# Kernel tuning notes

Measured on AMD Instinct MI355X. Metric: run time of the kernel, lower is better.

The kernel has to match this reference:

```python
import jax, jax.numpy as jnp
import numpy as np

TOP_K = 1
N_EXPERTS = 32
ALPHA = 0.001
SCALING = 1.0


def setup_inputs() -> dict:
    key = jax.random.key(0)
    k1, k2 = jax.random.split(key)
    hidden_states = jax.random.normal(k1, (16, 8192, 256), dtype=jnp.float32)
    # kaiming_uniform-ish gate weight, scale irrelevant for correctness check
    weight = jax.random.normal(k2, (32, 256), dtype=jnp.float32) * 0.06
    return {"hidden_states": hidden_states, "weight": weight}


def reference(hidden_states, weight):
    bsz, seq_len, h = hidden_states.shape
    x = hidden_states.reshape(-1, h).astype(jnp.float32)           # [N, h]
    logits = jnp.einsum('nh,eh->ne', x, weight.astype(jnp.float32))  # [N, E]
    scores = jax.nn.softmax(logits, axis=-1)
    # greedy top-k (sorted order fine; torch uses sorted=False but values identical for k=1)
    topk_weight, topk_idx = jax.lax.top_k(scores, TOP_K)            # [N, K]
    topk_weight = topk_weight * SCALING  # norm_topk_prob=False, top_k=1
    # seq_aux loss (training branch, alpha > 0)
    idx_aux = topk_idx.reshape(bsz, seq_len * TOP_K)                # [B, S*K]
    ce = jax.vmap(lambda idx: jnp.zeros((N_EXPERTS,), jnp.float32).at[idx].add(1.0))(idx_aux)
    ce = ce / (seq_len * TOP_K / N_EXPERTS)
    scores_seq = scores.reshape(bsz, seq_len, N_EXPERTS)
    aux_loss = jnp.mean(jnp.sum(ce * jnp.mean(scores_seq, axis=1), axis=1)) * ALPHA
    return topk_idx, topk_weight, aux_loss
```

## Files before the change

### kernel.cpp

```cpp
#include <hip/hip_runtime.h>
#include <math.h>

#define NTOK (16 * 8192)
#define H    256
#define E    32
#define SEQ  8192
#define BSZ  16

#define FOR_E(M) M(0) M(1) M(2) M(3) M(4) M(5) M(6) M(7) \
                 M(8) M(9) M(10) M(11) M(12) M(13) M(14) M(15) \
                 M(16) M(17) M(18) M(19) M(20) M(21) M(22) M(23) \
                 M(24) M(25) M(26) M(27) M(28) M(29) M(30) M(31)

__device__ __forceinline__ float waveReduceSum(float v) {
#pragma unroll
    for (int off = 32; off > 0; off >>= 1) v += __shfl_xor(v, off, 64);
    return v;
}

__global__ __launch_bounds__(256) void zero_ws_kernel(float* ws) {
    int i = blockIdx.x * 256 + threadIdx.x;
    if (i < BSZ * E * 2) ws[i] = 0.0f;
}

__global__ __launch_bounds__(256, 2) void gate_kernel(
    const float* __restrict__ x, const float* __restrict__ w,
    float* __restrict__ out, float* __restrict__ ws_cnt, float* __restrict__ ws_sum)
{
    __shared__ float w_lds[E * H];

    const int tid = threadIdx.x;

    {
        float4*       wl = (float4*)w_lds;
        const float4* wg = (const float4*)w;
#pragma unroll
        for (int i = 0; i < (E * H / 4) / 256; ++i)
            wl[tid + 256 * i] = wg[tid + 256 * i];
    }
    __syncthreads();

    const int lane = tid & 63;
    const int col  = lane & 31;
    const int half = lane >> 5;
    const int wavebase = blockIdx.x * 256 + (tid >> 6) * 64;
    const int tok0 = wavebase + col * 2;

    const float* xb = x + (size_t)tok0 * H + half * 128;
    const float* wb = w_lds + half * 128;

#define DECL_ACC(e) float aA##e = 0.0f, aB##e = 0.0f;
    FOR_E(DECL_ACC)

    float4 cA0 = *(const float4*)(xb);
    float4 cA1 = *(const float4*)(xb + 4);
    float4 cB0 = *(const float4*)(xb + H);
    float4 cB1 = *(const float4*)(xb + H + 4);

#pragma unroll 1
    for (int hc = 0; hc < 128; hc += 8) {
        const int hn = (hc + 8) & 127;
        const float4 nA0 = *(const float4*)(xb + hn);
        const float4 nA1 = *(const float4*)(xb + hn + 4);
        const float4 nB0 = *(const float4*)(xb + H + hn);
        const float4 nB1 = *(const float4*)(xb + H + hn + 4);

#define FMA_E(e) { \
        const float4 w0 = *(const float4*)(wb + (e) * H + hc); \
        const float4 w1 = *(const float4*)(wb + (e) * H + hc + 4); \
        float ta = aA##e, tb = aB##e; \
        ta = fmaf(w0.x, cA0.x, ta); ta = fmaf(w0.y, cA0.y, ta); \
        ta = fmaf(w0.z, cA0.z, ta); ta = fmaf(w0.w, cA0.w, ta); \
        ta = fmaf(w1.x, cA1.x, ta); ta = fmaf(w1.y, cA1.y, ta); \
        ta = fmaf(w1.z, cA1.z, ta); ta = fmaf(w1.w, cA1.w, ta); \
        tb = fmaf(w0.x, cB0.x, tb); tb = fmaf(w0.y, cB0.y, tb); \
        tb = fmaf(w0.z, cB0.z, tb); tb = fmaf(w0.w, cB0.w, tb); \
        tb = fmaf(w1.x, cB1.x, tb); tb = fmaf(w1.y, cB1.y, tb); \
        tb = fmaf(w1.z, cB1.z, tb); tb = fmaf(w1.w, cB1.w, tb); \
        aA##e = ta; aB##e = tb; }
        FOR_E(FMA_E)

        cA0 = nA0; cA1 = nA1; cB0 = nB0; cB1 = nB1;
    }

#define RED_E(e) aA##e += __shfl_xor(aA##e, 32, 64); aB##e += __shfl_xor(aB##e, 32, 64);
    FOR_E(RED_E)

#define SEL_E(e) const float L##e = half ? aB##e : aA##e;
    FOR_E(SEL_E)

    float m  = -3.402823466e+38f;
    int   id = 0;
#define AMAX_E(e) if (L##e > m) { m = L##e; id = (e); }
    FOR_E(AMAX_E)

    float ss = 0.0f;
#define EXP_E(e) const float p##e = __expf(L##e - m); ss += p##e;
    FOR_E(EXP_E)

    const float inv = 1.0f / ss;
    const int token = tok0 + half;
    out[token]        = (float)id;
    out[NTOK + token] = inv;

    const int b = wavebase >> 13;

#define AUX_E(e) { \
        const float sc = waveReduceSum(p##e * inv); \
        const unsigned long long bl = __ballot(id == (e)); \
        if (lane == 0) { \
            atomicAdd(&ws_sum[b * E + (e)], sc); \
            const float cn = (float)__popcll(bl); \
            if (cn != 0.0f) atomicAdd(&ws_cnt[b * E + (e)], cn); \
        } }
    FOR_E(AUX_E)
}

__global__ __launch_bounds__(256) void aux_kernel(
    const float* __restrict__ ws_cnt, const float* __restrict__ ws_sum,
    float* __restrict__ out)
{
    const int tid = threadIdx.x;
    float p = 0.0f;
    for (int i = tid; i < BSZ * E; i += 256)
        p += ws_cnt[i] * ws_sum[i];

    __shared__ float red[4];
#pragma unroll
    for (int off = 32; off > 0; off >>= 1)
        p += __shfl_xor(p, off, 64);
    if ((tid & 63) == 0) red[tid >> 6] = p;
    __syncthreads();
    if (tid == 0) {
        float t = red[0] + red[1] + red[2] + red[3];
        out[2 * NTOK] = t * (0.001f / (16.0f * 256.0f * 8192.0f));
    }
}

extern "C" void kernel_launch(void* const* d_in, const int* in_sizes, int n_in,
                              void* d_out, int out_size, void* d_ws, size_t ws_size,
                              hipStream_t stream) {
    const float* x = (const float*)d_in[0];
    const float* w = (const float*)d_in[1];
    float* out    = (float*)d_out;
    float* ws     = (float*)d_ws;
    float* ws_cnt = ws;
    float* ws_sum = ws + BSZ * E;

    zero_ws_kernel<<<4, 256, 0, stream>>>(ws);
    gate_kernel<<<NTOK / 256, 256, 0, stream>>>(x, w, out, ws_cnt, ws_sum);
    aux_kernel<<<1, 256, 0, stream>>>(ws_cnt, ws_sum, out);
}
```

Measured before the change: 261.4 us.

## Map one token per thread, read gate weights from global, aggregate aux stats in LDS

Each thread now computes the full 256-dim dot products for one token instead of splitting the hidden dimension across half-waves, which removes the cross-lane shuffle reduction. The gate weight is read straight from global memory (wave-uniform addresses, so likely scalar/cached loads) instead of being staged into 32KB of LDS, freeing LDS and raising possible occupancy. Per-block aux sums and counts are gathered in shared memory first, so each block issues only 32 global atomics per array. The trade-off is a strided per-thread row access pattern for x (each lane reads a different 1KB row), which may hurt coalescing, and a prefetch distance of 16 floats.

```diff
diff --git a/kernel.cpp b/kernel.cpp
--- a/kernel.cpp
+++ b/kernel.cpp
@@ -27,93 +27,74 @@
     const float* __restrict__ x, const float* __restrict__ w,
     float* __restrict__ out, float* __restrict__ ws_cnt, float* __restrict__ ws_sum)
 {
-    __shared__ float w_lds[E * H];
+    __shared__ float s_sum[E];
+    __shared__ float s_cnt[E];
 
-    const int tid = threadIdx.x;
+    const int tid   = threadIdx.x;
+    const int lane  = tid & 63;
+    const int token = blockIdx.x * 256 + tid;
+    const float* xb = x + (size_t)token * H;
 
-    {
-        float4*       wl = (float4*)w_lds;
-        const float4* wg = (const float4*)w;
-#pragma unroll
-        for (int i = 0; i < (E * H / 4) / 256; ++i)
-            wl[tid + 256 * i] = wg[tid + 256 * i];
-    }
+    if (tid < E) { s_sum[tid] = 0.0f; s_cnt[tid] = 0.0f; }
     __syncthreads();
 
-    const int lane = tid & 63;
-    const int col  = lane & 31;
-    const int half = lane >> 5;
-    const int wavebase = blockIdx.x * 256 + (tid >> 6) * 64;
-    const int tok0 = wavebase + col * 2;
-
-    const float* xb = x + (size_t)tok0 * H + half * 128;
-    const float* wb = w_lds + half * 128;
-
-#define DECL_ACC(e) float aA##e = 0.0f, aB##e = 0.0f;
+#define DECL_ACC(e) float a##e = 0.0f;
     FOR_E(DECL_ACC)
 
-    float4 cA0 = *(const float4*)(xb);
-    float4 cA1 = *(const float4*)(xb + 4);
-    float4 cB0 = *(const float4*)(xb + H);
-    float4 cB1 = *(const float4*)(xb + H + 4);
+    float4 c0 = *(const float4*)(xb);
+    float4 c1 = *(const float4*)(xb + 4);
+    float4 d0 = *(const float4*)(xb + 8);
+    float4 d1 = *(const float4*)(xb + 12);
 
 #pragma unroll 1
-    for (int hc = 0; hc < 128; hc += 8) {
-        const int hn = (hc + 8) & 127;
-        const float4 nA0 = *(const float4*)(xb + hn);
-        const float4 nA1 = *(const float4*)(xb + hn + 4);
-        const float4 nB0 = *(const float4*)(xb + H + hn);
-        const float4 nB1 = *(const float4*)(xb + H + hn + 4);
+    for (int hc = 0; hc < H; hc += 8) {
+        const int hn = (hc + 16) & (H - 1);
+        const float4 e0 = *(const float4*)(xb + hn);
+        const float4 e1 = *(const float4*)(xb + hn + 4);
 
 #define FMA_E(e) { \
-        const float4 w0 = *(const float4*)(wb + (e) * H + hc); \
-        const float4 w1 = *(const float4*)(wb + (e) * H + hc + 4); \
-        float ta = aA##e, tb = aB##e; \
-        ta = fmaf(w0.x, cA0.x, ta); ta = fmaf(w0.y, cA0.y, ta); \
-        ta = fmaf(w0.z, cA0.z, ta); ta = fmaf(w0.w, cA0.w, ta); \
-        ta = fmaf(w1.x, cA1.x, ta); ta = fmaf(w1.y, cA1.y, ta); \
-        ta = fmaf(w1.z, cA1.z, ta); ta = fmaf(w1.w, cA1.w, ta); \
-        tb = fmaf(w0.x, cB0.x, tb); tb = fmaf(w0.y, cB0.y, tb); \
-        tb = fmaf(w0.z, cB0.z, tb); tb = fmaf(w0.w, cB0.w, tb); \
-        tb = fmaf(w1.x, cB1.x, tb); tb = fmaf(w1.y, cB1.y, tb); \
-        tb = fmaf(w1.z, cB1.z, tb); tb = fmaf(w1.w, cB1.w, tb); \
-        aA##e = ta; aB##e = tb; }
+        const float4 w0 = *(const float4*)(w + (e) * H + hc); \
+        const float4 w1 = *(const float4*)(w + (e) * H + hc + 4); \
+        float t = a##e; \
+        t = fmaf(w0.x, c0.x, t); t = fmaf(w0.y, c0.y, t); \
+        t = fmaf(w0.z, c0.z, t); t = fmaf(w0.w, c0.w, t); \
+        t = fmaf(w1.x, c1.x, t); t = fmaf(w1.y, c1.y, t); \
+        t = fmaf(w1.z, c1.z, t); t = fmaf(w1.w, c1.w, t); \
+        a##e = t; }
         FOR_E(FMA_E)
 
-        cA0 = nA0; cA1 = nA1; cB0 = nB0; cB1 = nB1;
+        c0 = d0; c1 = d1; d0 = e0; d1 = e1;
     }
-
-#define RED_E(e) aA##e += __shfl_xor(aA##e, 32, 64); aB##e += __shfl_xor(aB##e, 32, 64);
-    FOR_E(RED_E)
-
-#define SEL_E(e) const float L##e = half ? aB##e : aA##e;
-    FOR_E(SEL_E)
 
     float m  = -3.402823466e+38f;
     int   id = 0;
-#define AMAX_E(e) if (L##e > m) { m = L##e; id = (e); }
+#define AMAX_E(e) if (a##e > m) { m = a##e; id = (e); }
     FOR_E(AMAX_E)
 
     float ss = 0.0f;
-#define EXP_E(e) const float p##e = __expf(L##e - m); ss += p##e;
+#define EXP_E(e) const float p##e = __expf(a##e - m); ss += p##e;
     FOR_E(EXP_E)
 
     const float inv = 1.0f / ss;
-    const int token = tok0 + half;
     out[token]        = (float)id;
     out[NTOK + token] = inv;
-
-    const int b = wavebase >> 13;
 
 #define AUX_E(e) { \
         const float sc = waveReduceSum(p##e * inv); \
         const unsigned long long bl = __ballot(id == (e)); \
         if (lane == 0) { \
-            atomicAdd(&ws_sum[b * E + (e)], sc); \
-            const float cn = (float)__popcll(bl); \
-            if (cn != 0.0f) atomicAdd(&ws_cnt[b * E + (e)], cn); \
+            atomicAdd(&s_sum[(e)], sc); \
+            if (bl) atomicAdd(&s_cnt[(e)], (float)__popcll(bl)); \
         } }
     FOR_E(AUX_E)
+
+    __syncthreads();
+    if (tid < E) {
+        const int b = blockIdx.x >> 5;
+        atomicAdd(&ws_sum[b * E + tid], s_sum[tid]);
+        const float cn = s_cnt[tid];
+        if (cn != 0.0f) atomicAdd(&ws_cnt[b * E + tid], cn);
+    }
 }
 
 __global__ __launch_bounds__(256) void aux_kernel(
```

Result: slower. 341.3 us (+30.6%).
